# Performance work log

Measured on AMD Instinct MI355X. Metric: run time of the kernel, lower is better.

## Reference

```python
import jax, jax.numpy as jnp
import numpy as np

D_MODEL = 1024
N_HEAD = 16


def setup_inputs() -> dict:
    key = jax.random.key(0)
    ks = jax.random.split(key, 12)
    B, S, D = 4, 2048, D_MODEL
    scale = 1.0 / np.sqrt(D)
    inp = {
        "Q": jax.random.normal(ks[0], (B, S, D), jnp.float32),
        "K": jax.random.normal(ks[1], (B, S, D), jnp.float32),
        "V": jax.random.normal(ks[2], (B, S, D), jnp.float32),
        "Wq": jax.random.normal(ks[3], (D, D), jnp.float32) * scale,
        "bq": jax.random.normal(ks[4], (D,), jnp.float32) * scale,
        "Wk": jax.random.normal(ks[5], (D, D), jnp.float32) * scale,
        "bk": jax.random.normal(ks[6], (D,), jnp.float32) * scale,
        "Wv": jax.random.normal(ks[7], (D, D), jnp.float32) * scale,
        "bv": jax.random.normal(ks[8], (D,), jnp.float32) * scale,
        "Wo": jax.random.normal(ks[9], (D, D), jnp.float32) * scale,
        "bo": jax.random.normal(ks[10], (D,), jnp.float32) * scale,
    }
    return inp


def _split_heads(x, n_head):
    B, S, D = x.shape
    return x.reshape(B, S, n_head, D // n_head).transpose(0, 2, 1, 3)  # [B,H,S,dh]


def reference(Q, K, V, Wq, bq, Wk, bk, Wv, bv, Wo, bo):
    # torch Linear: x @ W.T + b
    q = _split_heads(Q @ Wq.T + bq, N_HEAD)
    k = _split_heads(K @ Wk.T + bk, N_HEAD)
    v = _split_heads(V @ Wv.T + bv, N_HEAD)
    d_k = k.shape[-1]
    score = jnp.einsum('bhqd,bhkd->bhqk', q, k) / jnp.sqrt(jnp.float32(d_k))
    attn = jax.nn.softmax(score, axis=-1)
    out = jnp.einsum('bhqk,bhkd->bhqd', attn, v)  # [B,H,S,dh]
    B, H, S, dh = out.shape
    out = out.transpose(0, 2, 1, 3).reshape(B, S, H * dh)
    return out @ Wo.T + bo
```

## Files before the change

### kernel.cpp

```cpp
#include <hip/hip_runtime.h>
#include <math.h>

#define D_MODEL 1024
#define N_HEAD  16
#define DH      64
#define SEQ     2048
#define BATCH   4
#define BH      (BATCH*N_HEAD)
#define MROWS   (BATCH*SEQ)

typedef __attribute__((ext_vector_type(8)))  short          s16x8;
typedef __attribute__((ext_vector_type(8)))  unsigned short u16x8;
typedef __attribute__((ext_vector_type(4)))  unsigned short u16x4;
typedef __attribute__((ext_vector_type(4)))  float          f32x4;
typedef __attribute__((ext_vector_type(16))) float          f32x16;
typedef __attribute__((ext_vector_type(4)))  unsigned int   u32x4;

#define QSCALE 0.18033688f

__device__ __forceinline__ unsigned short f2bf(float x) {
    unsigned int u = __float_as_uint(x);
    u += 0x7FFFu + ((u >> 16) & 1u);
    return (unsigned short)(u >> 16);
}

__device__ __forceinline__ unsigned int cvtpk_bf16(float lo, float hi) {
    unsigned int r;
    asm("v_cvt_pk_bf16_f32 %0, %1, %2" : "=v"(r) : "v"(lo), "v"(hi));
    return r;
}

__device__ __forceinline__ float exp2_asm(float x) {
    float r;
    asm("v_exp_f32 %0, %1" : "=v"(r) : "v"(x));
    return r;
}

__global__ __launch_bounds__(256) void conv_w4(const float* __restrict__ w0,
                                               const float* __restrict__ w1,
                                               const float* __restrict__ w2,
                                               const float* __restrict__ w3,
                                               unsigned short* __restrict__ o0,
                                               unsigned short* __restrict__ o1,
                                               unsigned short* __restrict__ o2,
                                               unsigned short* __restrict__ o3)
{
    const float* w; unsigned short* o;
    switch (blockIdx.y) {
        case 0:  w = w0; o = o0; break;
        case 1:  w = w1; o = o1; break;
        case 2:  w = w2; o = o2; break;
        default: w = w3; o = o3; break;
    }
    int i = blockIdx.x * 256 + threadIdx.x;
    const float4* p = (const float4*)w + (size_t)i * 2;
    float4 a = p[0], b = p[1];
    u16x8 v;
    v[0] = f2bf(a.x); v[1] = f2bf(a.y); v[2] = f2bf(a.z); v[3] = f2bf(a.w);
    v[4] = f2bf(b.x); v[5] = f2bf(b.y); v[6] = f2bf(b.z); v[7] = f2bf(b.w);
    *((u16x8*)o + i) = v;
}

template<int MODE, bool AF32>
__global__ __launch_bounds__(256) void gemm_bt(const void* __restrict__ Av,
                                               const unsigned short* __restrict__ W,
                                               const float* __restrict__ bias,
                                               unsigned short* __restrict__ outb,
                                               float* __restrict__ outf,
                                               float oscale)
{
    __shared__ short As[128 * 64];
    __shared__ short Bs[128 * 64];
    const int tid = threadIdx.x;
    const int w = tid >> 6, l = tid & 63;
    const int lr = l & 15, lg = l >> 4;
    const int wm = w >> 1, wn = w & 1;
    const int r0 = blockIdx.x * 128, c0 = blockIdx.y * 128;
    const int srow = tid >> 3;
    const int sc8  = tid & 7;

    f32x4 zz = {0.f, 0.f, 0.f, 0.f};
    f32x4 acc[4][4];
    #pragma unroll
    for (int i = 0; i < 4; ++i)
        #pragma unroll
        for (int j = 0; j < 4; ++j) acc[i][j] = zz;

    const unsigned short* Ab = (const unsigned short*)Av;
    const float*          Af = (const float*)Av;

    u16x8 ar[4], br[4];
    float4 arf[4][2];
    #pragma unroll
    for (int p = 0; p < 4; ++p) {
        int row = p * 32 + srow;
        if (AF32) {
            arf[p][0] = *(const float4*)(Af + (size_t)(r0 + row) * 1024 + sc8 * 8);
            arf[p][1] = *(const float4*)(Af + (size_t)(r0 + row) * 1024 + sc8 * 8 + 4);
        } else {
            ar[p] = *(const u16x8*)(Ab + (size_t)(r0 + row) * 1024 + sc8 * 8);
        }
        br[p] = *(const u16x8*)(W + (size_t)(c0 + row) * 1024 + sc8 * 8);
    }

    for (int ks = 0; ks < 16; ++ks) {
        __syncthreads();
        #pragma unroll
        for (int p = 0; p < 4; ++p) {
            int row = p * 32 + srow;
            if (AF32) {
                u32x4 wd;
                wd[0] = cvtpk_bf16(arf[p][0].x, arf[p][0].y);
                wd[1] = cvtpk_bf16(arf[p][0].z, arf[p][0].w);
                wd[2] = cvtpk_bf16(arf[p][1].x, arf[p][1].y);
                wd[3] = cvtpk_bf16(arf[p][1].z, arf[p][1].w);
                *(u16x8*)&As[row * 64 + ((sc8 ^ (row & 7)) * 8)] = __builtin_bit_cast(u16x8, wd);
            } else {
                *(u16x8*)&As[row * 64 + ((sc8 ^ (row & 7)) * 8)] = ar[p];
            }
            *(u16x8*)&Bs[row * 64 + ((sc8 ^ (row & 7)) * 8)] = br[p];
        }
        __syncthreads();
        if (ks < 15) {
            int k0 = (ks + 1) * 64;
            #pragma unroll
            for (int p = 0; p < 4; ++p) {
                int row = p * 32 + srow;
                if (AF32) {
                    arf[p][0] = *(const float4*)(Af + (size_t)(r0 + row) * 1024 + k0 + sc8 * 8);
                    arf[p][1] = *(const float4*)(Af + (size_t)(r0 + row) * 1024 + k0 + sc8 * 8 + 4);
                } else {
                    ar[p] = *(const u16x8*)(Ab + (size_t)(r0 + row) * 1024 + k0 + sc8 * 8);
                }
                br[p] = *(const u16x8*)(W + (size_t)(c0 + row) * 1024 + k0 + sc8 * 8);
            }
        }
        #pragma unroll
        for (int t = 0; t < 2; ++t) {
            const int k8 = lg + 4 * t;
            s16x8 af[4], bw[4];
            #pragma unroll
            for (int i = 0; i < 4; ++i) {
                int rowa = wm * 64 + i * 16 + lr;
                af[i] = *(const s16x8*)&As[rowa * 64 + ((k8 ^ (rowa & 7)) * 8)];
                int rowb = wn * 64 + i * 16 + lr;
                bw[i] = *(const s16x8*)&Bs[rowb * 64 + ((k8 ^ (rowb & 7)) * 8)];
            }
            #pragma unroll
            for (int i = 0; i < 4; ++i)
                #pragma unroll
                for (int j = 0; j < 4; ++j)
                    acc[i][j] = __builtin_amdgcn_mfma_f32_16x16x32_bf16(af[i], bw[j], acc[i][j], 0, 0, 0);
        }
    }

    #pragma unroll
    for (int i = 0; i < 4; ++i) {
        #pragma unroll
        for (int j = 0; j < 4; ++j) {
            const int colb = c0 + wn * 64 + j * 16 + lr;
            const float bv = bias[colb];
            if (MODE == 2) {
                const int row = r0 + wm * 64 + i * 16 + lg * 4;
                const int b = row >> 11, s = row & 2047;
                const int h = colb >> 6, d = colb & 63;
                u16x4 pv;
                pv[0] = f2bf((acc[i][j][0] + bv) * oscale);
                pv[1] = f2bf((acc[i][j][1] + bv) * oscale);
                pv[2] = f2bf((acc[i][j][2] + bv) * oscale);
                pv[3] = f2bf((acc[i][j][3] + bv) * oscale);
                *(u16x4*)(outb + ((size_t)(b * N_HEAD + h) * DH + d) * SEQ + s) = pv;
            } else {
                #pragma unroll
                for (int rg = 0; rg < 4; ++rg) {
                    const int row = r0 + wm * 64 + i * 16 + lg * 4 + rg;
                    const float v = acc[i][j][rg] + bv;
                    if (MODE == 0) {
                        outf[(size_t)row * D_MODEL + colb] = v;
                    } else {
                        const int b = row >> 11, s = row & 2047;
                        const int h = colb >> 6, d = colb & 63;
                        outb[((size_t)(b * N_HEAD + h) * SEQ + s) * DH + d] = f2bf(v * oscale);
                    }
                }
            }
        }
    }
}

__global__ __launch_bounds__(256) void flash_attn_mfma32(const unsigned short* __restrict__ qb,
                                                         const unsigned short* __restrict__ kb,
                                                         const unsigned short* __restrict__ vtb,
                                                         unsigned short* __restrict__ aob)
{
    __shared__ u16x8 Kt[512];
    __shared__ u16x8 Vt[512];

    const int tid = threadIdx.x;
    const int w = tid >> 6, l = tid & 63;
    const int q32 = l & 31;
    const int h = l >> 5;
    const int qt = blockIdx.x, bh = blockIdx.y;
    const unsigned short* qh = qb + (size_t)bh * SEQ * DH;
    const unsigned short* kh = kb + (size_t)bh * SEQ * DH;
    const unsigned short* vh = vtb + (size_t)bh * DH * SEQ;

    const int qrow = qt * 128 + w * 32 + q32;

    s16x8 qf[4];
    #pragma unroll
    for (int ks = 0; ks < 4; ++ks)
        qf[ks] = *(const s16x8*)(qh + (size_t)qrow * DH + ks * 16 + h * 8);

    f32x16 O[2];
    #pragma unroll
    for (int c = 0; c < 2; ++c)
        #pragma unroll
        for (int r = 0; r < 16; ++r) O[c][r] = 0.f;
    float m = -1e30f, lsum = 0.f;

    const int srow = tid >> 3;
    const int sc8  = tid & 7;

    u16x8 kreg[2], vreg[2];
    #pragma unroll
    for (int p = 0; p < 2; ++p) {
        int rr = p * 32 + srow;
        kreg[p] = *(const u16x8*)(kh + (size_t)rr * DH + sc8 * 8);
        vreg[p] = *(const u16x8*)(vh + (size_t)rr * SEQ + sc8 * 8);
    }

    for (int kv = 0; kv < SEQ / 64; ++kv) {
        __syncthreads();
        #pragma unroll
        for (int p = 0; p < 2; ++p) {
            int rr = p * 32 + srow;
            Kt[sc8 * 64 + (rr ^ sc8)] = kreg[p];
            Vt[sc8 * 64 + (rr ^ sc8)] = vreg[p];
        }
        __syncthreads();
        if (kv < SEQ / 64 - 1) {
            const int s0 = (kv + 1) * 64;
            #pragma unroll
            for (int p = 0; p < 2; ++p) {
                int rr = p * 32 + srow;
                kreg[p] = *(const u16x8*)(kh + (size_t)(s0 + rr) * DH + sc8 * 8);
                vreg[p] = *(const u16x8*)(vh + (size_t)rr * SEQ + s0 + sc8 * 8);
            }
        }

        f32x16 SC[2];
        #pragma unroll
        for (int c = 0; c < 2; ++c)
            #pragma unroll
            for (int r = 0; r < 16; ++r) SC[c][r] = 0.f;
        #pragma unroll
        for (int ks = 0; ks < 4; ++ks) {
            const int chunk = 2 * ks + h;
            #pragma unroll
            for (int c = 0; c < 2; ++c) {
                const int row = c * 32 + q32;
                s16x8 kf = __builtin_bit_cast(s16x8, Kt[chunk * 64 + (row ^ chunk)]);
                SC[c] = __builtin_amdgcn_mfma_f32_32x32x16_bf16(kf, qf[ks], SC[c], 0, 0, 0);
            }
        }

        float t0[8];
        #pragma unroll
        for (int r = 0; r < 8; ++r)
            t0[r] = fmaxf(fmaxf(SC[0][r], SC[0][r + 8]), fmaxf(SC[1][r], SC[1][r + 8]));
        #pragma unroll
        for (int d = 4; d; d >>= 1)
            #pragma unroll
            for (int r = 0; r < d; ++r) t0[r] = fmaxf(t0[r], t0[r + d]);
        float rm = fmaxf(t0[0], __shfl_xor(t0[0], 32, 64));

        if (!__all(rm - m <= 8.0f)) {
            const float nm = fmaxf(m, rm);
            const float fold = exp2_asm(m - nm);
            lsum *= fold;
            O[0] *= fold;
            O[1] *= fold;
            m = nm;
        }

        #pragma unroll
        for (int c = 0; c < 2; ++c)
            #pragma unroll
            for (int r = 0; r < 16; ++r)
                SC[c][r] = exp2_asm(SC[c][r] - m);

        float s0a[8];
        #pragma unroll
        for (int r = 0; r < 8; ++r)
            s0a[r] = (SC[0][r] + SC[0][r + 8]) + (SC[1][r] + SC[1][r + 8]);
        #pragma unroll
        for (int d = 4; d; d >>= 1)
            #pragma unroll
            for (int r = 0; r < d; ++r) s0a[r] += s0a[r + d];
        lsum += s0a[0] + __shfl_xor(s0a[0], 32, 64);

        s16x8 pa[4];
        #pragma unroll
        for (int s = 0; s < 4; ++s) {
            const int c = s >> 1, rb = (s & 1) * 8;
            unsigned int a0 = cvtpk_bf16(SC[c][rb + 0], SC[c][rb + 1]);
            unsigned int a1 = cvtpk_bf16(SC[c][rb + 2], SC[c][rb + 3]);
            unsigned int b0 = cvtpk_bf16(SC[c][rb + 4], SC[c][rb + 5]);
            unsigned int b1 = cvtpk_bf16(SC[c][rb + 6], SC[c][rb + 7]);
            unsigned int x0 = (unsigned int)__shfl_xor((int)a0, 32, 64);
            unsigned int x1 = (unsigned int)__shfl_xor((int)a1, 32, 64);
            unsigned int y0 = (unsigned int)__shfl_xor((int)b0, 32, 64);
            unsigned int y1 = (unsigned int)__shfl_xor((int)b1, 32, 64);
            u32x4 wd;
            wd[0] = h ? y0 : a0;
            wd[1] = h ? y1 : a1;
            wd[2] = h ? b0 : x0;
            wd[3] = h ? b1 : x1;
            pa[s] = __builtin_bit_cast(s16x8, wd);
        }

        #pragma unroll
        for (int s = 0; s < 4; ++s) {
            const int chunk = 2 * s + h;
            #pragma unroll
            for (int c = 0; c < 2; ++c) {
                const int row = c * 32 + q32;
                s16x8 vf = __builtin_bit_cast(s16x8, Vt[chunk * 64 + (row ^ chunk)]);
                O[c] = __builtin_amdgcn_mfma_f32_32x32x16_bf16(vf, pa[s], O[c], 0, 0, 0);
            }
        }
    }

    const float inv = 1.0f / lsum;
    const int b = bh >> 4, head = bh & 15;
    unsigned short* obase = aob + ((size_t)b * SEQ + qrow) * D_MODEL + head * DH;
    #pragma unroll
    for (int c = 0; c < 2; ++c) {
        #pragma unroll
        for (int rq = 0; rq < 4; ++rq) {
            const int d0 = 8 * rq + 4 * h + 32 * c;
            u16x4 pv;
            #pragma unroll
            for (int j = 0; j < 4; ++j) pv[j] = f2bf(O[c][rq * 4 + j] * inv);
            *(u16x4*)(obase + d0) = pv;
        }
    }
}

extern "C" void kernel_launch(void* const* d_in, const int* in_sizes, int n_in,
                              void* d_out, int out_size, void* d_ws, size_t ws_size,
                              hipStream_t stream)
{
    const float* Q  = (const float*)d_in[0];
    const float* K  = (const float*)d_in[1];
    const float* V  = (const float*)d_in[2];
    const float* Wq = (const float*)d_in[3];
    const float* bq = (const float*)d_in[4];
    const float* Wk = (const float*)d_in[5];
    const float* bk = (const float*)d_in[6];
    const float* Wv = (const float*)d_in[7];
    const float* bv = (const float*)d_in[8];
    const float* Wo = (const float*)d_in[9];
    const float* bo = (const float*)d_in[10];

    const size_t PER = (size_t)MROWS * D_MODEL;
    const size_t WSZ = (size_t)D_MODEL * D_MODEL;
    unsigned short* wqb = (unsigned short*)d_ws;
    unsigned short* wkb = wqb + WSZ;
    unsigned short* wvb = wkb + WSZ;
    unsigned short* wob = wvb + WSZ;
    unsigned short* qb2 = wob + WSZ;
    unsigned short* kb2 = qb2 + PER;
    unsigned short* vtb = kb2 + PER;
    unsigned short* aob = vtb + PER;

    dim3 gg(MROWS / 128, D_MODEL / 128);

    conv_w4<<<dim3(512, 4), 256, 0, stream>>>(Wq, Wk, Wv, Wo, wqb, wkb, wvb, wob);

    gemm_bt<1, true><<<gg, 256, 0, stream>>>(Q, wqb, bq, qb2, nullptr, QSCALE);
    gemm_bt<1, true><<<gg, 256, 0, stream>>>(K, wkb, bk, kb2, nullptr, 1.0f);
    gemm_bt<2, true><<<gg, 256, 0, stream>>>(V, wvb, bv, vtb, nullptr, 1.0f);

    flash_attn_mfma32<<<dim3(SEQ / 128, BH), 256, 0, stream>>>(qb2, kb2, vtb, aob);

    gemm_bt<0, false><<<gg, 256, 0, stream>>>(aob, wob, bo, nullptr, (float*)d_out, 1.0f);
}
```

Measured before the change: 245.5 us.

## Double-buffer K/V LDS in flash attention, fold max into MFMA seed, XCD-aware block mapping

```diff
diff --git a/kernel.cpp b/kernel.cpp
--- a/kernel.cpp
+++ b/kernel.cpp
@@ -188,19 +188,25 @@
     }
 }
 
-__global__ __launch_bounds__(256) void flash_attn_mfma32(const unsigned short* __restrict__ qb,
-                                                         const unsigned short* __restrict__ kb,
-                                                         const unsigned short* __restrict__ vtb,
-                                                         unsigned short* __restrict__ aob)
+__global__ __launch_bounds__(256, 4) void flash_attn_mfma32(const unsigned short* __restrict__ qb,
+                                                            const unsigned short* __restrict__ kb,
+                                                            const unsigned short* __restrict__ vtb,
+                                                            unsigned short* __restrict__ aob)
 {
-    __shared__ u16x8 Kt[512];
-    __shared__ u16x8 Vt[512];
+    __shared__ u16x8 Kt[2][512];
+    __shared__ u16x8 Vt[2][512];
 
     const int tid = threadIdx.x;
     const int w = tid >> 6, l = tid & 63;
     const int q32 = l & 31;
     const int h = l >> 5;
-    const int qt = blockIdx.x, bh = blockIdx.y;
+
+    const int wg   = blockIdx.x;
+    const int xcd  = wg & 7;
+    const int slot = wg >> 3;
+    const int bh   = xcd * 8 + (slot >> 4);
+    const int qt   = slot & 15;
+
     const unsigned short* qh = qb + (size_t)bh * SEQ * DH;
     const unsigned short* kh = kb + (size_t)bh * SEQ * DH;
     const unsigned short* vh = vtb + (size_t)bh * DH * SEQ;
@@ -217,7 +223,7 @@
     for (int c = 0; c < 2; ++c)
         #pragma unroll
         for (int r = 0; r < 16; ++r) O[c][r] = 0.f;
-    float m = -1e30f, lsum = 0.f;
+    float m = 0.f, lsum = 0.f;
 
     const int srow = tid >> 3;
     const int sc8  = tid & 7;
@@ -229,16 +235,16 @@
         kreg[p] = *(const u16x8*)(kh + (size_t)rr * DH + sc8 * 8);
         vreg[p] = *(const u16x8*)(vh + (size_t)rr * SEQ + sc8 * 8);
     }
-
+    #pragma unroll
+    for (int p = 0; p < 2; ++p) {
+        int rr = p * 32 + srow;
+        Kt[0][sc8 * 64 + (rr ^ sc8)] = kreg[p];
+        Vt[0][sc8 * 64 + (rr ^ sc8)] = vreg[p];
+    }
+    __syncthreads();
+
+    int buf = 0;
     for (int kv = 0; kv < SEQ / 64; ++kv) {
-        __syncthreads();
-        #pragma unroll
-        for (int p = 0; p < 2; ++p) {
-            int rr = p * 32 + srow;
-            Kt[sc8 * 64 + (rr ^ sc8)] = kreg[p];
-            Vt[sc8 * 64 + (rr ^ sc8)] = vreg[p];
-        }
-        __syncthreads();
         if (kv < SEQ / 64 - 1) {
             const int s0 = (kv + 1) * 64;
             #pragma unroll
@@ -249,46 +255,53 @@
             }
         }
 
+        f32x16 seed;
+        #pragma unroll
+        for (int r = 0; r < 16; ++r) seed[r] = -m;
         f32x16 SC[2];
-        #pragma unroll
-        for (int c = 0; c < 2; ++c)
-            #pragma unroll
-            for (int r = 0; r < 16; ++r) SC[c][r] = 0.f;
+        SC[0] = seed; SC[1] = seed;
+        __builtin_amdgcn_s_setprio(1);
         #pragma unroll
         for (int ks = 0; ks < 4; ++ks) {
             const int chunk = 2 * ks + h;
             #pragma unroll
             for (int c = 0; c < 2; ++c) {
                 const int row = c * 32 + q32;
-                s16x8 kf = __builtin_bit_cast(s16x8, Kt[chunk * 64 + (row ^ chunk)]);
+                s16x8 kf = __builtin_bit_cast(s16x8, Kt[buf][chunk * 64 + (row ^ chunk)]);
                 SC[c] = __builtin_amdgcn_mfma_f32_32x32x16_bf16(kf, qf[ks], SC[c], 0, 0, 0);
             }
         }
+        __builtin_amdgcn_s_setprio(0);
 
         float t0[8];
         #pragma unroll
         for (int r = 0; r < 8; ++r)
-            t0[r] = fmaxf(fmaxf(SC[0][r], SC[0][r + 8]), fmaxf(SC[1][r], SC[1][r + 8]));
+            t0[r] = fmaxf(fmaxf(fmaxf(SC[0][r], SC[0][r + 8]), SC[1][r]), SC[1][r + 8]);
         #pragma unroll
         for (int d = 4; d; d >>= 1)
             #pragma unroll
             for (int r = 0; r < d; ++r) t0[r] = fmaxf(t0[r], t0[r + d]);
-        float rm = fmaxf(t0[0], __shfl_xor(t0[0], 32, 64));
-
-        if (!__all(rm - m <= 8.0f)) {
-            const float nm = fmaxf(m, rm);
-            const float fold = exp2_asm(m - nm);
+        float rmb = fmaxf(t0[0], __shfl_xor(t0[0], 32, 64));
+
+        if (!__all(rmb <= 8.0f)) {
+            const float delta = fmaxf(rmb, 0.f);
+            const float fold = exp2_asm(-delta);
             lsum *= fold;
             O[0] *= fold;
             O[1] *= fold;
-            m = nm;
+            m += delta;
+            #pragma unroll
+            for (int c = 0; c < 2; ++c)
+                #pragma unroll
+                for (int r = 0; r < 16; ++r)
+                    SC[c][r] -= delta;
         }
 
         #pragma unroll
         for (int c = 0; c < 2; ++c)
             #pragma unroll
             for (int r = 0; r < 16; ++r)
-                SC[c][r] = exp2_asm(SC[c][r] - m);
+                SC[c][r] = exp2_asm(SC[c][r]);
 
         float s0a[8];
         #pragma unroll
@@ -320,15 +333,28 @@
             pa[s] = __builtin_bit_cast(s16x8, wd);
         }
 
+        __builtin_amdgcn_s_setprio(1);
         #pragma unroll
         for (int s = 0; s < 4; ++s) {
             const int chunk = 2 * s + h;
             #pragma unroll
             for (int c = 0; c < 2; ++c) {
                 const int row = c * 32 + q32;
-                s16x8 vf = __builtin_bit_cast(s16x8, Vt[chunk * 64 + (row ^ chunk)]);
+                s16x8 vf = __builtin_bit_cast(s16x8, Vt[buf][chunk * 64 + (row ^ chunk)]);
                 O[c] = __builtin_amdgcn_mfma_f32_32x32x16_bf16(vf, pa[s], O[c], 0, 0, 0);
             }
+        }
+        __builtin_amdgcn_s_setprio(0);
+
+        if (kv < SEQ / 64 - 1) {
+            #pragma unroll
+            for (int p = 0; p < 2; ++p) {
+                int rr = p * 32 + srow;
+                Kt[buf ^ 1][sc8 * 64 + (rr ^ sc8)] = kreg[p];
+                Vt[buf ^ 1][sc8 * 64 + (rr ^ sc8)] = vreg[p];
+            }
+            __syncthreads();
+            buf ^= 1;
         }
     }
 
@@ -383,7 +409,7 @@
     gemm_bt<1, true><<<gg, 256, 0, stream>>>(K, wkb, bk, kb2, nullptr, 1.0f);
     gemm_bt<2, true><<<gg, 256, 0, stream>>>(V, wvb, bv, vtb, nullptr, 1.0f);
 
-    flash_attn_mfma32<<<dim3(SEQ / 128, BH), 256, 0, stream>>>(qb2, kb2, vtb, aob);
+    flash_attn_mfma32<<<dim3(16 * BH), 256, 0, stream>>>(qb2, kb2, vtb, aob);
 
     gemm_bt<0, false><<<gg, 256, 0, stream>>>(aob, wob, bo, nullptr, (float*)d_out, 1.0f);
 }
```

Result: faster. 227.4 us (-7.4%).
